# Kernel tuning notes

Hardware: AMD Instinct MI355X
Metric: run time of the kernel (lower is better)

## Reference

```python
import jax, jax.numpy as jnp
import numpy as np

B, P = 65536, 22  # sets, max players per freeze frame
IN, HID, OUT = 6, 64, 128


def setup_inputs() -> dict:
    key = jax.random.key(0)
    k0, k1, k2, k3, k4, k5 = jax.random.split(key, 6)
    pitch = jnp.array([120.0, 80.0], dtype=jnp.float32)
    player_locs = jax.random.uniform(k0, (B, P, 2), dtype=jnp.float32) * pitch
    actor_locs = jax.random.uniform(k1, (B, 2), dtype=jnp.float32) * pitch
    # teammate / keeper flags in {0,1}
    flags = jax.random.randint(k2, (B, P, 2), 0, 2).astype(jnp.float32)
    # validity mask: 0 -> player skipped (simulates ragged / missing entries)
    mask = jax.random.randint(k3, (B, P), 0, 2).astype(jnp.int32)
    W1 = jax.random.normal(k4, (IN, HID), dtype=jnp.float32) / np.sqrt(IN)
    b1 = jnp.zeros((HID,), dtype=jnp.float32)
    W2 = jax.random.normal(k5, (HID, OUT), dtype=jnp.float32) / np.sqrt(HID)
    b2 = jnp.zeros((OUT,), dtype=jnp.float32)
    return {"player_locs": player_locs, "actor_locs": actor_locs, "flags": flags,
            "mask": mask, "W1": W1, "b1": b1, "W2": W2, "b2": b2}


def reference(player_locs, actor_locs, flags, mask, W1, b1, W2, b2):
    # per-player features relative to the actor: [dx, dy, dist, angle, teammate, keeper]
    dxy = player_locs - actor_locs[:, None, :]                 # [B,P,2]
    dist = jnp.sqrt(jnp.sum(dxy * dxy, axis=-1, keepdims=True))  # [B,P,1]
    angle = jnp.arctan2(dxy[..., 1:2], dxy[..., 0:1])            # [B,P,1]
    feats = jnp.concatenate([dxy, dist, angle, flags], axis=-1)  # [B,P,6]
    # PlayerMLP: Linear -> ReLU -> Linear
    h = jax.nn.relu(jnp.einsum('bpi,ih->bph', feats, W1) + b1)   # [B,P,64]
    emb = jnp.einsum('bph,ho->bpo', h, W2) + b2                  # [B,P,128]
    # masked mean over valid players; empty sets yield zeros (sum is 0)
    m = mask.astype(emb.dtype)[..., None]                        # [B,P,1]
    cnt = jnp.sum(m, axis=1)                                     # [B,1]
    pooled = jnp.sum(emb * m, axis=1) / jnp.maximum(cnt, 1.0)    # [B,128]
    return pooled
```

## Files before the change

### kernel.cpp

```cpp
#include <hip/hip_runtime.h>
#include <math.h>

#define PMAX 22
#define HID 64
#define OUTD 128
#define SETS_PER_WAVE 8
#define WAVES_PER_BLOCK 4
#define CHUNKS 2

typedef __attribute__((ext_vector_type(4))) float float4v;
typedef _Float16 fh2 __attribute__((ext_vector_type(2)));
typedef _Float16 half8 __attribute__((ext_vector_type(8)));

__device__ __forceinline__ int rl_i(int v, int l) {
    return __builtin_amdgcn_readlane(v, l);
}
__device__ __forceinline__ int pk2(float x, float y) {
    auto v = __builtin_amdgcn_cvt_pkrtz(x, y);
    union { decltype(v) h; int i; } c;
    c.h = v;
    return c.i;
}
__device__ __forceinline__ unsigned short f16b(float x) {
    return (unsigned short)(pk2(x, x) & 0xFFFF);
}
__device__ __forceinline__ float fdot2i(int a, int b, float c) {
    union { int i; fh2 h; } ua, ub;
    ua.i = a;
    ub.i = b;
#if defined(__has_builtin) && __has_builtin(__builtin_amdgcn_fdot2)
    return __builtin_amdgcn_fdot2(ua.h, ub.h, c, false);
#else
    return fmaf((float)ua.h.x, (float)ub.h.x, fmaf((float)ua.h.y, (float)ub.h.y, c));
#endif
}
__device__ __forceinline__ void wave_lds_sync() {
    asm volatile("s_waitcnt lgkmcnt(0)" ::: "memory");
    __builtin_amdgcn_wave_barrier();
}
__device__ __forceinline__ float fast_atan2(float y, float x) {
    float ax = fabsf(x), ay = fabsf(y);
    float mn = fminf(ax, ay), mx = fmaxf(ax, ay);
    float a = mn * __builtin_amdgcn_rcpf(fmaxf(mx, 1e-30f));
    float s = a * a;
    float r = a * fmaf(s, fmaf(s, fmaf(s, -0.0851330f, 0.1801410f), -0.3302995f), 0.9998660f);
    if (ay > ax) r = 1.57079637f - r;
    if (x < 0.0f) r = 3.14159274f - r;
    return copysignf(r, y);
}

__device__ __forceinline__ void prefetch_raw(
    const float* __restrict__ player_locs, const float* __restrict__ flags,
    const int* __restrict__ mask, const float* __restrict__ actor_locs,
    int set0, int lidx, float2 pl[4], float2 fl[4], float2 ac[4], int mk[4])
{
    const size_t r0 = (size_t)set0 * PMAX + lidx;
    const float2* plb = (const float2*)player_locs + r0;
    const float2* flb = (const float2*)flags + r0;
    const int*    mkb = mask + r0;
    const float2* acb = (const float2*)actor_locs + set0 + (lidx >= PMAX ? 1 : 0);
#pragma unroll
    for (int g = 0; g < 4; ++g) {
        pl[g] = plb[g * 2 * PMAX];
        fl[g] = flb[g * 2 * PMAX];
        mk[g] = mkb[g * 2 * PMAX];
        ac[g] = acb[2 * g];
    }
}

__global__ __launch_bounds__(256, 4) void set_encoder_kernel(
    const float* __restrict__ player_locs,
    const float* __restrict__ actor_locs,
    const float* __restrict__ flags,
    const int*   __restrict__ mask,
    const float* __restrict__ W1,
    const float* __restrict__ b1,
    const float* __restrict__ W2,
    const float* __restrict__ b2,
    float* __restrict__ out)
{
    __shared__ __align__(16) unsigned w2f[16 * 256];
    __shared__ __align__(16) unsigned short hb[WAVES_PER_BLOCK][SETS_PER_WAVE][72];

    const int tid  = threadIdx.x;
    const int lane = tid & 63;
    const int wave = tid >> 6;

    const int bset = blockIdx.x * (CHUNKS * WAVES_PER_BLOCK * SETS_PER_WAVE);

    const int pr  = tid >> 3;
    const int nt8 = tid & 7;
    float ra[16], rb[16];
    {
        const float* rA = W2 + (size_t)(2 * pr) * OUTD + 16 * nt8;
        const float* rB = rA + OUTD;
#pragma unroll
        for (int i = 0; i < 4; ++i) {
            *(float4*)&ra[4 * i] = ((const float4*)rA)[i];
            *(float4*)&rb[4 * i] = ((const float4*)rB)[i];
        }
    }

    const int lidx = lane < 2 * PMAX ? lane : 2 * PMAX - 1;
    float2 pl[4], fl[4], ac2[4];
    int    mk[4];
    prefetch_raw(player_locs, flags, mask, actor_locs,
                 bset + wave * SETS_PER_WAVE, lidx, pl, fl, ac2, mk);

    const int w01 = pk2(W1[0 * HID + lane], W1[1 * HID + lane]);
    const int w23 = pk2(W1[2 * HID + lane], W1[3 * HID + lane]);
    const int w45 = pk2(W1[4 * HID + lane], W1[5 * HID + lane]);
    const float b1l = b1[lane];

    const int c15 = lane & 15;
    const int Q   = lane >> 4;
    const int sA  = lane & 7;
    const int sq  = Q & 1;
    const int nh  = lane >> 5;
    float b2v[4];
#pragma unroll
    for (int k = 0; k < 4; ++k) b2v[k] = b2[64 * nh + 16 * k + c15];

    {
        const int kt = pr >> 4;
        const int kk = (2 * pr) & 31;
        const int Qs = kk >> 3;
        const int j2 = (kk >> 1) & 3;
        const int sbase = ((kt * 8 + nt8) * 4 + Qs) * 64 + j2;
#pragma unroll
        for (int c = 0; c < 16; ++c)
            w2f[sbase + 4 * c] = pk2(ra[c], rb[c]);
    }

    __syncthreads();

#pragma unroll
    for (int c = 0; c < CHUNKS; ++c) {
        const int set0 = bset + c * (WAVES_PER_BLOCK * SETS_PER_WAVE) + wave * SETS_PER_WAVE;

        int fh[4][3];
        unsigned long long wbm[4];
#pragma unroll
        for (int g = 0; g < 4; ++g) {
            float dx = pl[g].x - ac2[g].x;
            float dy = pl[g].y - ac2[g].y;
            float dist = __builtin_amdgcn_sqrtf(fmaf(dx, dx, dy * dy));
            float ang  = fast_atan2(dy, dx);
            fh[g][0] = pk2(dx, dy);
            fh[g][1] = pk2(dist, ang);
            fh[g][2] = pk2(fl[g].x, fl[g].y);
            unsigned long long bl = __ballot((lane < 2 * PMAX) && (mk[g] != 0));
            const unsigned lo = __builtin_amdgcn_readfirstlane((unsigned)bl);
            const unsigned hi = __builtin_amdgcn_readfirstlane((unsigned)(bl >> 32));
            wbm[g] = ((unsigned long long)hi << 32) | lo;
        }

        if (c + 1 < CHUNKS)
            prefetch_raw(player_locs, flags, mask, actor_locs,
                         bset + (c + 1) * (WAVES_PER_BLOCK * SETS_PER_WAVE) + wave * SETS_PER_WAVE,
                         lidx, pl, fl, ac2, mk);

        unsigned nonempty = 0;
#pragma unroll
        for (int s = 0; s < SETS_PER_WAVE; ++s) {
            const int g    = s >> 1;
            const int base = (s & 1) * PMAX;
            const unsigned bits = (unsigned)(wbm[g] >> base) & 0x3FFFFFu;
            const int cnt = __builtin_popcount(bits);
            if (bits) nonempty |= (1u << s);
            float accv = 0.0f;
#pragma unroll
            for (int p = 0; p < PMAX; ++p) {
                if (bits & (1u << p)) {
                    float t = fdot2i(rl_i(fh[g][0], base + p), w01, b1l);
                    t = fdot2i(rl_i(fh[g][1], base + p), w23, t);
                    t = fdot2i(rl_i(fh[g][2], base + p), w45, t);
                    accv += fmaxf(t, 0.0f);
                }
            }
            const float hbar = accv * __builtin_amdgcn_rcpf(fmaxf((float)cnt, 1.0f));
            hb[wave][s][lane] = f16b(hbar);
        }
        wave_lds_sync();

        half8 afrag[2];
#pragma unroll
        for (int kt = 0; kt < 2; ++kt) {
            union { uint4 u4; half8 h8; } cv;
            cv.u4 = *(const uint4*)&hb[wave][sA][kt * 32 + Q * 8];
            afrag[kt] = cv.h8;
        }

        float4v acc[8];
#pragma unroll
        for (int nt = 0; nt < 8; ++nt) {
            union { uint4 u4; half8 h8; } f0, f1;
            f0.u4 = *(const uint4*)&w2f[(0 * 8 + nt) * 256 + 4 * lane];
            f1.u4 = *(const uint4*)&w2f[(1 * 8 + nt) * 256 + 4 * lane];
            float4v z = {0.0f, 0.0f, 0.0f, 0.0f};
            acc[nt] = __builtin_amdgcn_mfma_f32_16x16x32_f16(afrag[0], f0.h8, z, 0, 0, 0);
            acc[nt] = __builtin_amdgcn_mfma_f32_16x16x32_f16(afrag[1], f1.h8, acc[nt], 0, 0, 0);
        }

        float fs[4];
#pragma unroll
        for (int r = 0; r < 4; ++r) fs[r] = (float)((nonempty >> (4 * sq + r)) & 1u);

        float* obase = out + (size_t)(set0 + 4 * sq) * OUTD + 64 * nh + c15;
#pragma unroll
        for (int k = 0; k < 4; ++k) {
            float4v av = nh ? acc[4 + k] : acc[k];
#pragma unroll
            for (int r = 0; r < 4; ++r)
                obase[r * OUTD + 16 * k] = fmaf(fs[r], b2v[k], av[r]);
        }
    }
}

extern "C" void kernel_launch(void* const* d_in, const int* in_sizes, int n_in,
                              void* d_out, int out_size, void* d_ws, size_t ws_size,
                              hipStream_t stream) {
    const float* player_locs = (const float*)d_in[0];
    const float* actor_locs  = (const float*)d_in[1];
    const float* flags       = (const float*)d_in[2];
    const int*   mask        = (const int*)d_in[3];
    const float* W1          = (const float*)d_in[4];
    const float* b1          = (const float*)d_in[5];
    const float* W2          = (const float*)d_in[6];
    const float* b2          = (const float*)d_in[7];
    float*       out         = (float*)d_out;

    const int B = in_sizes[0] / (PMAX * 2);
    const int sets_per_block = CHUNKS * WAVES_PER_BLOCK * SETS_PER_WAVE;
    const int grid = (B + sets_per_block - 1) / sets_per_block;

    hipLaunchKernelGGL(set_encoder_kernel, dim3(grid), dim3(256), 0, stream,
                       player_locs, actor_locs, flags, mask, W1, b1, W2, b2, out);
}
```

Baseline: 120.0 us.

## Drop chunked prefetch loop and XOR-swizzle W2 fragments in LDS

```diff
diff --git a/kernel.cpp b/kernel.cpp
--- a/kernel.cpp
+++ b/kernel.cpp
@@ -6,7 +6,6 @@
 #define OUTD 128
 #define SETS_PER_WAVE 8
 #define WAVES_PER_BLOCK 4
-#define CHUNKS 2
 
 typedef __attribute__((ext_vector_type(4))) float float4v;
 typedef _Float16 fh2 __attribute__((ext_vector_type(2)));
@@ -49,26 +48,7 @@
     return copysignf(r, y);
 }
 
-__device__ __forceinline__ void prefetch_raw(
-    const float* __restrict__ player_locs, const float* __restrict__ flags,
-    const int* __restrict__ mask, const float* __restrict__ actor_locs,
-    int set0, int lidx, float2 pl[4], float2 fl[4], float2 ac[4], int mk[4])
-{
-    const size_t r0 = (size_t)set0 * PMAX + lidx;
-    const float2* plb = (const float2*)player_locs + r0;
-    const float2* flb = (const float2*)flags + r0;
-    const int*    mkb = mask + r0;
-    const float2* acb = (const float2*)actor_locs + set0 + (lidx >= PMAX ? 1 : 0);
-#pragma unroll
-    for (int g = 0; g < 4; ++g) {
-        pl[g] = plb[g * 2 * PMAX];
-        fl[g] = flb[g * 2 * PMAX];
-        mk[g] = mkb[g * 2 * PMAX];
-        ac[g] = acb[2 * g];
-    }
-}
-
-__global__ __launch_bounds__(256, 4) void set_encoder_kernel(
+__global__ __launch_bounds__(256) void set_encoder_kernel(
     const float* __restrict__ player_locs,
     const float* __restrict__ actor_locs,
     const float* __restrict__ flags,
@@ -86,7 +66,8 @@
     const int lane = tid & 63;
     const int wave = tid >> 6;
 
-    const int bset = blockIdx.x * (CHUNKS * WAVES_PER_BLOCK * SETS_PER_WAVE);
+    const int wave_id = blockIdx.x * WAVES_PER_BLOCK + wave;
+    const int set0    = wave_id * SETS_PER_WAVE;
 
     const int pr  = tid >> 3;
     const int nt8 = tid & 7;
@@ -104,8 +85,20 @@
     const int lidx = lane < 2 * PMAX ? lane : 2 * PMAX - 1;
     float2 pl[4], fl[4], ac2[4];
     int    mk[4];
-    prefetch_raw(player_locs, flags, mask, actor_locs,
-                 bset + wave * SETS_PER_WAVE, lidx, pl, fl, ac2, mk);
+    {
+        const size_t r0 = (size_t)set0 * PMAX + lidx;
+        const float2* plb = (const float2*)player_locs + r0;
+        const float2* flb = (const float2*)flags + r0;
+        const int*    mkb = mask + r0;
+        const float2* acb = (const float2*)actor_locs + set0 + (lidx >= PMAX ? 1 : 0);
+#pragma unroll
+        for (int g = 0; g < 4; ++g) {
+            pl[g]  = plb[g * 2 * PMAX];
+            fl[g]  = flb[g * 2 * PMAX];
+            mk[g]  = mkb[g * 2 * PMAX];
+            ac2[g] = acb[2 * g];
+        }
+    }
 
     const int w01 = pk2(W1[0 * HID + lane], W1[1 * HID + lane]);
     const int w23 = pk2(W1[2 * HID + lane], W1[3 * HID + lane]);
@@ -126,94 +119,86 @@
         const int kk = (2 * pr) & 31;
         const int Qs = kk >> 3;
         const int j2 = (kk >> 1) & 3;
-        const int sbase = ((kt * 8 + nt8) * 4 + Qs) * 64 + j2;
-#pragma unroll
-        for (int c = 0; c < 16; ++c)
-            w2f[sbase + 4 * c] = pk2(ra[c], rb[c]);
+        const int tb = (kt * 8 + nt8) * 256;
+#pragma unroll
+        for (int c = 0; c < 16; ++c) {
+            const int u = (Qs * 16 + c) ^ nt8;
+            w2f[tb + u * 4 + j2] = pk2(ra[c], rb[c]);
+        }
     }
 
     __syncthreads();
 
-#pragma unroll
-    for (int c = 0; c < CHUNKS; ++c) {
-        const int set0 = bset + c * (WAVES_PER_BLOCK * SETS_PER_WAVE) + wave * SETS_PER_WAVE;
-
-        int fh[4][3];
-        unsigned long long wbm[4];
-#pragma unroll
-        for (int g = 0; g < 4; ++g) {
-            float dx = pl[g].x - ac2[g].x;
-            float dy = pl[g].y - ac2[g].y;
-            float dist = __builtin_amdgcn_sqrtf(fmaf(dx, dx, dy * dy));
-            float ang  = fast_atan2(dy, dx);
-            fh[g][0] = pk2(dx, dy);
-            fh[g][1] = pk2(dist, ang);
-            fh[g][2] = pk2(fl[g].x, fl[g].y);
-            unsigned long long bl = __ballot((lane < 2 * PMAX) && (mk[g] != 0));
-            const unsigned lo = __builtin_amdgcn_readfirstlane((unsigned)bl);
-            const unsigned hi = __builtin_amdgcn_readfirstlane((unsigned)(bl >> 32));
-            wbm[g] = ((unsigned long long)hi << 32) | lo;
-        }
-
-        if (c + 1 < CHUNKS)
-            prefetch_raw(player_locs, flags, mask, actor_locs,
-                         bset + (c + 1) * (WAVES_PER_BLOCK * SETS_PER_WAVE) + wave * SETS_PER_WAVE,
-                         lidx, pl, fl, ac2, mk);
-
-        unsigned nonempty = 0;
-#pragma unroll
-        for (int s = 0; s < SETS_PER_WAVE; ++s) {
-            const int g    = s >> 1;
-            const int base = (s & 1) * PMAX;
-            const unsigned bits = (unsigned)(wbm[g] >> base) & 0x3FFFFFu;
-            const int cnt = __builtin_popcount(bits);
-            if (bits) nonempty |= (1u << s);
-            float accv = 0.0f;
-#pragma unroll
-            for (int p = 0; p < PMAX; ++p) {
-                if (bits & (1u << p)) {
-                    float t = fdot2i(rl_i(fh[g][0], base + p), w01, b1l);
-                    t = fdot2i(rl_i(fh[g][1], base + p), w23, t);
-                    t = fdot2i(rl_i(fh[g][2], base + p), w45, t);
-                    accv += fmaxf(t, 0.0f);
-                }
+    int fh[4][3];
+    unsigned long long wbm[4];
+#pragma unroll
+    for (int g = 0; g < 4; ++g) {
+        float dx = pl[g].x - ac2[g].x;
+        float dy = pl[g].y - ac2[g].y;
+        float dist = __builtin_amdgcn_sqrtf(fmaf(dx, dx, dy * dy));
+        float ang  = fast_atan2(dy, dx);
+        fh[g][0] = pk2(dx, dy);
+        fh[g][1] = pk2(dist, ang);
+        fh[g][2] = pk2(fl[g].x, fl[g].y);
+        unsigned long long bl = __ballot((lane < 2 * PMAX) && (mk[g] != 0));
+        const unsigned lo = __builtin_amdgcn_readfirstlane((unsigned)bl);
+        const unsigned hi = __builtin_amdgcn_readfirstlane((unsigned)(bl >> 32));
+        wbm[g] = ((unsigned long long)hi << 32) | lo;
+    }
+
+    unsigned nonempty = 0;
+#pragma unroll
+    for (int s = 0; s < SETS_PER_WAVE; ++s) {
+        const int g    = s >> 1;
+        const int base = (s & 1) * PMAX;
+        const unsigned bits = (unsigned)(wbm[g] >> base) & 0x3FFFFFu;
+        const int cnt = __builtin_popcount(bits);
+        if (bits) nonempty |= (1u << s);
+        float accv = 0.0f;
+#pragma unroll
+        for (int p = 0; p < PMAX; ++p) {
+            if (bits & (1u << p)) {
+                float t = fdot2i(rl_i(fh[g][0], base + p), w01, b1l);
+                t = fdot2i(rl_i(fh[g][1], base + p), w23, t);
+                t = fdot2i(rl_i(fh[g][2], base + p), w45, t);
+                accv += fmaxf(t, 0.0f);
             }
-            const float hbar = accv * __builtin_amdgcn_rcpf(fmaxf((float)cnt, 1.0f));
-            hb[wave][s][lane] = f16b(hbar);
-        }
-        wave_lds_sync();
-
-        half8 afrag[2];
-#pragma unroll
-        for (int kt = 0; kt < 2; ++kt) {
-            union { uint4 u4; half8 h8; } cv;
-            cv.u4 = *(const uint4*)&hb[wave][sA][kt * 32 + Q * 8];
-            afrag[kt] = cv.h8;
-        }
-
-        float4v acc[8];
-#pragma unroll
-        for (int nt = 0; nt < 8; ++nt) {
-            union { uint4 u4; half8 h8; } f0, f1;
-            f0.u4 = *(const uint4*)&w2f[(0 * 8 + nt) * 256 + 4 * lane];
-            f1.u4 = *(const uint4*)&w2f[(1 * 8 + nt) * 256 + 4 * lane];
-            float4v z = {0.0f, 0.0f, 0.0f, 0.0f};
-            acc[nt] = __builtin_amdgcn_mfma_f32_16x16x32_f16(afrag[0], f0.h8, z, 0, 0, 0);
-            acc[nt] = __builtin_amdgcn_mfma_f32_16x16x32_f16(afrag[1], f1.h8, acc[nt], 0, 0, 0);
-        }
-
-        float fs[4];
-#pragma unroll
-        for (int r = 0; r < 4; ++r) fs[r] = (float)((nonempty >> (4 * sq + r)) & 1u);
-
-        float* obase = out + (size_t)(set0 + 4 * sq) * OUTD + 64 * nh + c15;
-#pragma unroll
-        for (int k = 0; k < 4; ++k) {
-            float4v av = nh ? acc[4 + k] : acc[k];
-#pragma unroll
-            for (int r = 0; r < 4; ++r)
-                obase[r * OUTD + 16 * k] = fmaf(fs[r], b2v[k], av[r]);
-        }
+        }
+        const float hbar = accv * __builtin_amdgcn_rcpf(fmaxf((float)cnt, 1.0f));
+        hb[wave][s][lane] = f16b(hbar);
+    }
+    wave_lds_sync();
+
+    half8 afrag[2];
+#pragma unroll
+    for (int kt = 0; kt < 2; ++kt) {
+        union { uint4 u4; half8 h8; } cv;
+        cv.u4 = *(const uint4*)&hb[wave][sA][kt * 32 + Q * 8];
+        afrag[kt] = cv.h8;
+    }
+
+    float4v acc[8];
+#pragma unroll
+    for (int nt = 0; nt < 8; ++nt) {
+        union { uint4 u4; half8 h8; } f0, f1;
+        f0.u4 = *(const uint4*)&w2f[(0 * 8 + nt) * 256 + 4 * (lane ^ nt)];
+        f1.u4 = *(const uint4*)&w2f[(1 * 8 + nt) * 256 + 4 * (lane ^ nt)];
+        float4v z = {0.0f, 0.0f, 0.0f, 0.0f};
+        acc[nt] = __builtin_amdgcn_mfma_f32_16x16x32_f16(afrag[0], f0.h8, z, 0, 0, 0);
+        acc[nt] = __builtin_amdgcn_mfma_f32_16x16x32_f16(afrag[1], f1.h8, acc[nt], 0, 0, 0);
+    }
+
+    float fs[4];
+#pragma unroll
+    for (int r = 0; r < 4; ++r) fs[r] = (float)((nonempty >> (4 * sq + r)) & 1u);
+
+    float* obase = out + (size_t)(set0 + 4 * sq) * OUTD + 64 * nh + c15;
+#pragma unroll
+    for (int k = 0; k < 4; ++k) {
+        float4v av = nh ? acc[4 + k] : acc[k];
+#pragma unroll
+        for (int r = 0; r < 4; ++r)
+            obase[r * OUTD + 16 * k] = fmaf(fs[r], b2v[k], av[r]);
     }
 }
 
@@ -231,7 +216,7 @@
     float*       out         = (float*)d_out;
 
     const int B = in_sizes[0] / (PMAX * 2);
-    const int sets_per_block = CHUNKS * WAVES_PER_BLOCK * SETS_PER_WAVE;
+    const int sets_per_block = WAVES_PER_BLOCK * SETS_PER_WAVE;
     const int grid = (B + sets_per_block - 1) / sets_per_block;
 
     hipLaunchKernelGGL(set_encoder_kernel, dim3(grid), dim3(256), 0, stream,
```

Measured after the change: 122.4 us. 1.02x slower.
